# Performance work log

Measured on AMD Instinct MI355X. Metric: run time of the kernel, lower is better.

Reference implementation:

```python
import jax, jax.numpy as jnp
import numpy as np

N, E, D, H, C = 50000, 1600000, 128, 2, 32

def setup_inputs() -> dict:
    key = jax.random.key(0)
    ks = jax.random.split(key, 8)
    x = jax.random.normal(ks[0], (N, D), jnp.float32)
    edge_index = jax.random.randint(ks[1], (2, E), 0, N)
    intra_enrichment_weights = jax.random.uniform(ks[2], (E,), jnp.float32)
    W = jax.random.normal(ks[3], (D, H * C), jnp.float32) * (1.0 / np.sqrt(D))
    att_src = jax.random.normal(ks[4], (H, C), jnp.float32) * 0.1
    att_dst = jax.random.normal(ks[5], (H, C), jnp.float32) * 0.1
    bias = jnp.zeros((H * C,), jnp.float32)
    enrichment_scale = jnp.asarray(0.01, jnp.float32)
    return dict(x=x, edge_index=edge_index,
                intra_enrichment_weights=intra_enrichment_weights,
                W=W, att_src=att_src, att_dst=att_dst, bias=bias,
                enrichment_scale=enrichment_scale)

def reference(x, edge_index, intra_enrichment_weights, W, att_src, att_dst, bias, enrichment_scale):
    n = x.shape[0]
    xf = jax.nn.elu(x)                       # F.elu on input features
    h = (xf @ W).reshape(n, H, C)            # [N, heads, out]
    # GATConv default add_self_loops=True
    loop = jnp.arange(n, dtype=edge_index.dtype)
    src = jnp.concatenate([edge_index[0], loop])
    dst = jnp.concatenate([edge_index[1], loop])
    a_src = jnp.einsum('nhc,hc->nh', h, att_src)   # [N, H]
    a_dst = jnp.einsum('nhc,hc->nh', h, att_dst)
    alpha = jax.nn.leaky_relu(a_src[src] + a_dst[dst], 0.2)  # [E+N, H]
    # softmax over incoming edges per destination node
    m = jax.ops.segment_max(alpha, dst, num_segments=n)
    e = jnp.exp(alpha - m[dst])
    denom = jax.ops.segment_sum(e, dst, num_segments=n)
    p = e / denom[dst]                       # every node has a self-loop -> denom > 0
    out = jax.ops.segment_sum(h[src] * p[:, :, None], dst, num_segments=n)  # [N, H, C]
    out = out.reshape(n, H * C) + bias
    # enrichment bias (scatter-mean of per-edge weights over source nodes)
    s0 = edge_index[0]
    nw = jax.ops.segment_sum(intra_enrichment_weights, s0, num_segments=n)
    cnt = jax.ops.segment_sum(jnp.ones_like(intra_enrichment_weights), s0, num_segments=n)
    nw = nw / jnp.maximum(cnt, 1.0)
    nw = jnp.clip(nw, 0.2, 5.0)
    scale_factor = 0.1 * jax.nn.sigmoid(enrichment_scale)
    return out + scale_factor * (nw[:, None] - 1.0)
```

## Files before the change

kernel.cpp:

```cpp
#include <hip/hip_runtime.h>


typedef unsigned int u32;
typedef unsigned short u16;

#define SLOTS 4864
#define NB_MAX 400
#define EPB 4096

#define XS 136
#define CS 68

#define SMEM_F 43392

typedef __attribute__((ext_vector_type(8))) short short8;
typedef __attribute__((ext_vector_type(4))) float float4v;

__device__ __forceinline__ u16 f2bf(float f) {
    union { float f; u32 u; } v; v.f = f;
    u32 r = v.u + 0x7fffu + ((v.u >> 16) & 1u);
    return (u16)(r >> 16);
}
__device__ __forceinline__ float bf2f(u16 u) {
    union { u32 i; float f; } v; v.i = ((u32)u) << 16; return v.f;
}
__device__ __forceinline__ float bf_lo(u32 u) {
    union { u32 i; float f; } v; v.i = u << 16; return v.f;
}
__device__ __forceinline__ float bf_hi(u32 u) {
    union { u32 i; float f; } v; v.i = u & 0xFFFF0000u; return v.f;
}
__device__ __forceinline__ void bf_split(float v, short& hi, short& lo) {
    u16 h = f2bf(v);
    float hf = bf2f(h);
    hi = (short)h;
    lo = (short)f2bf(v - hf);
}

__global__ void k_prep(const float* __restrict__ Wm,
                       short* __restrict__ Whf, short* __restrict__ Wlf,
                       int* cursA, int* cursB)
{
    int t = threadIdx.x;
    for (int i = t; i < NB_MAX; i += 256) { cursA[i] = 0; cursB[i] = 0; }
    for (int p = t; p < 1024; p += 256) {
        int frag = p >> 6, l = p & 63;
        int ks = frag >> 2, nt = frag & 3;
        int q = l >> 4, m = l & 15;
        int f = nt * 16 + m;
#pragma unroll
        for (int j = 0; j < 8; ++j) {
            int k = ks * 32 + q * 8 + j;
            float wv = Wm[k * 64 + f];
            short hi, lo; bf_split(wv, hi, lo);
            Whf[p * 8 + j] = hi;
            Wlf[p * 8 + j] = lo;
        }
    }
}

static __device__ __forceinline__ void node_body(
    char* smem, int nb_id,
    const float* __restrict__ x,
    const short* __restrict__ Whf, const short* __restrict__ Wlf,
    const float* __restrict__ att_s, const float* __restrict__ att_d,
    u32* __restrict__ hb32, float* __restrict__ a_src, float* __restrict__ a_dst,
    int nN)
{
    short* Ah = (short*)smem;
    short* Al = (short*)(smem + 17408);
    float* Cl = (float*)Ah;

    int t = threadIdx.x;
    int n0 = nb_id * 64;

    for (int j = 0; j < 8; ++j) {
        int idx = t + 256 * j;
        int r = idx >> 5, c4 = idx & 31;
        int gn = n0 + r;
        float4 xv = make_float4(0.f, 0.f, 0.f, 0.f);
        if (gn < nN) xv = ((const float4*)x)[(size_t)gn * 32 + c4];
        float e[4];
        e[0] = xv.x > 0.f ? xv.x : __expf(xv.x) - 1.f;
        e[1] = xv.y > 0.f ? xv.y : __expf(xv.y) - 1.f;
        e[2] = xv.z > 0.f ? xv.z : __expf(xv.z) - 1.f;
        e[3] = xv.w > 0.f ? xv.w : __expf(xv.w) - 1.f;
        short h4[4], l4[4];
#pragma unroll
        for (int i = 0; i < 4; ++i) bf_split(e[i], h4[i], l4[i]);
        *(short4*)&Ah[r * XS + c4 * 4] = make_short4(h4[0], h4[1], h4[2], h4[3]);
        *(short4*)&Al[r * XS + c4 * 4] = make_short4(l4[0], l4[1], l4[2], l4[3]);
    }
    __syncthreads();

    {
        int w = t >> 6, l = t & 63;
        int q = l >> 4, m = l & 15;
        int arow = w * 16 + m;
        float4v acc[4] = {};
#pragma unroll
        for (int ks = 0; ks < 4; ++ks) {
            int k0 = ks * 32 + q * 8;
            short8 ah = *(const short8*)&Ah[arow * XS + k0];
            short8 al = *(const short8*)&Al[arow * XS + k0];
#pragma unroll
            for (int nt = 0; nt < 4; ++nt) {
                short8 bh = *(const short8*)&Whf[((ks * 4 + nt) * 64 + l) * 8];
                short8 bl = *(const short8*)&Wlf[((ks * 4 + nt) * 64 + l) * 8];
                acc[nt] = __builtin_amdgcn_mfma_f32_16x16x32_bf16(ah, bh, acc[nt], 0, 0, 0);
                acc[nt] = __builtin_amdgcn_mfma_f32_16x16x32_bf16(ah, bl, acc[nt], 0, 0, 0);
                acc[nt] = __builtin_amdgcn_mfma_f32_16x16x32_bf16(al, bh, acc[nt], 0, 0, 0);
            }
        }
        __syncthreads();
#pragma unroll
        for (int nt = 0; nt < 4; ++nt)
#pragma unroll
            for (int r = 0; r < 4; ++r)
                Cl[(w * 16 + q * 4 + r) * CS + nt * 16 + m] = acc[nt][r];
    }
    __syncthreads();

    {
        int nl = t >> 2, fq = t & 3;
        int gn = n0 + nl;
        float ps = 0.f, pd = 0.f;
        if (gn < nN) {
            float hv[16];
#pragma unroll
            for (int i = 0; i < 16; ++i) {
                int f = fq * 16 + i;
                hv[i] = Cl[nl * CS + f];
                ps = fmaf(hv[i], att_s[f], ps);
                pd = fmaf(hv[i], att_d[f], pd);
            }
#pragma unroll
            for (int i = 0; i < 8; ++i) {
                u32 pk = ((u32)f2bf(hv[2 * i + 1]) << 16) | (u32)f2bf(hv[2 * i]);
                hb32[(size_t)gn * 32 + fq * 8 + i] = pk;
            }
        }
        float ps2 = ps + __shfl_xor(ps, 1, 64);
        float pd2 = pd + __shfl_xor(pd, 1, 64);
        if (gn < nN && (fq & 1) == 0) {
            a_src[2 * gn + (fq >> 1)] = ps2;
            a_dst[2 * gn + (fq >> 1)] = pd2;
        }
    }
}

static __device__ __forceinline__ void partA_body(
    char* smem, int pa_id,
    const int* __restrict__ ei, const float* __restrict__ wgt,
    int* cursA, int* cursB, u32* bufA, u32* bufB, int E, int nb)
{
    u32* arrA  = (u32*)smem;
    u32* arrB  = (u32*)(smem + 16384);
    int* cntA  = (int*)(smem + 32768);
    int* cntB  = (int*)(smem + 34368);
    int* lofsA = (int*)(smem + 35968);
    int* lofsB = (int*)(smem + 37568);
    int* basA  = (int*)(smem + 39168);
    int* basB  = (int*)(smem + 40768);
    int* part  = (int*)(smem + 42368);

    int t = threadIdx.x;
    for (int b = t; b < nb; b += 256) { cntA[b] = 0; cntB[b] = 0; }
    __syncthreads();

    int base = pa_id * EPB;
    int nv = min(EPB, E - base);
    int sv[16], dv[16]; float wv[16];
#pragma unroll
    for (int k = 0; k < 16; ++k) {
        int e = base + k * 256 + t;
        if (e < E) { sv[k] = ei[e]; dv[k] = ei[E + e]; wv[k] = wgt[e]; }
        else       { sv[k] = -1;    dv[k] = -1;        wv[k] = 0.f; }
    }
#pragma unroll
    for (int k = 0; k < 16; ++k) {
        if (dv[k] >= 0) {
            atomicAdd(&cntA[dv[k] >> 7], 1);
            atomicAdd(&cntB[sv[k] >> 7], 1);
        }
    }
    __syncthreads();
    for (int b = t; b < nb; b += 256) {
        int ca = cntA[b], cb = cntB[b];
        if (ca > 0) basA[b] = atomicAdd(&cursA[b], ca);
        if (cb > 0) basB[b] = atomicAdd(&cursB[b], cb);
    }
    __syncthreads();
    {
        int b0 = 2 * t, b1 = 2 * t + 1;
        int c0 = (b0 < nb) ? cntA[b0] : 0;
        int c1 = (b1 < nb) ? cntA[b1] : 0;
        part[t] = c0 + c1;
        __syncthreads();
        for (int off = 1; off < 256; off <<= 1) {
            int v = (t >= off) ? part[t - off] : 0;
            __syncthreads();
            part[t] += v;
            __syncthreads();
        }
        int excl = part[t] - (c0 + c1);
        if (b0 < nb) lofsA[b0] = excl;
        if (b1 < nb) lofsA[b1] = excl + c0;
        __syncthreads();
        c0 = (b0 < nb) ? cntB[b0] : 0;
        c1 = (b1 < nb) ? cntB[b1] : 0;
        part[t] = c0 + c1;
        __syncthreads();
        for (int off = 1; off < 256; off <<= 1) {
            int v = (t >= off) ? part[t - off] : 0;
            __syncthreads();
            part[t] += v;
            __syncthreads();
        }
        excl = part[t] - (c0 + c1);
        if (b0 < nb) lofsB[b0] = excl;
        if (b1 < nb) lofsB[b1] = excl + c0;
    }
    __syncthreads();
    for (int b = t; b < nb; b += 256) { cntA[b] = 0; cntB[b] = 0; }
    __syncthreads();
#pragma unroll
    for (int k = 0; k < 16; ++k) {
        if (dv[k] >= 0) {
            int bA = dv[k] >> 7;
            int r = lofsA[bA] + atomicAdd(&cntA[bA], 1);
            arrA[r] = ((u32)bA << 23) | ((u32)(dv[k] & 127) << 16) | (u32)sv[k];
            int bB = sv[k] >> 7;
            u32 wf = (u32)(wv[k] * 65536.f);
            if (wf > 0xFFFFu) wf = 0xFFFFu;
            int r2 = lofsB[bB] + atomicAdd(&cntB[bB], 1);
            arrB[r2] = ((u32)bB << 23) | ((u32)(sv[k] & 127) << 16) | wf;
        }
    }
    __syncthreads();
    for (int i = t; i < nv; i += 256) {
        u32 va = arrA[i];
        int bA = va >> 23;
        int g = basA[bA] + (i - lofsA[bA]);
        if (g < SLOTS) bufA[bA * SLOTS + g] = va & 0x7FFFFFu;
        u32 vb = arrB[i];
        int bB = vb >> 23;
        int g2 = basB[bB] + (i - lofsB[bB]);
        if (g2 < SLOTS) bufB[bB * SLOTS + g2] = vb & 0x7FFFFFu;
    }
}

__global__ __launch_bounds__(256) void k_fused(
    const float* __restrict__ x,
    const short* __restrict__ Whf, const short* __restrict__ Wlf,
    const float* __restrict__ att_s, const float* __restrict__ att_d,
    u32* __restrict__ hb32, float* __restrict__ a_src, float* __restrict__ a_dst,
    const int* __restrict__ ei, const float* __restrict__ wgt,
    int* cursA, int* cursB, u32* bufA, u32* bufB,
    int E, int nb, int nblkA, int nN)
{
    __shared__ __align__(16) char smem[SMEM_F];
    int bid = blockIdx.x;
    int q3 = bid / 3;
    if ((bid % 3) == 0 && q3 < nblkA) {
        partA_body(smem, q3, ei, wgt, cursA, cursB, bufA, bufB, E, nb);
    } else {
        int npa_before = min(q3 + ((bid % 3) ? 1 : 0), nblkA);
        node_body(smem, bid - npa_before, x, Whf, Wlf, att_s, att_d,
                  hb32, a_src, a_dst, nN);
    }
}

__global__ __launch_bounds__(1024) void k_final(
    const u32* __restrict__ hb32,
    const float* __restrict__ a_src, const float* __restrict__ a_dst,
    const u32* __restrict__ bufA, const int* __restrict__ cursA,
    const u32* __restrict__ bufB, const int* __restrict__ cursB,
    const float* __restrict__ bias, const float* __restrict__ esc,
    float* __restrict__ out, int nN)
{
    __shared__ u32 st[SLOTS];
    __shared__ u16 st2[SLOTS];
    __shared__ int ldeg[128], lscan[128], lcur[128];
    __shared__ u32 usum[128];
    __shared__ int ucnt[128];

    int b = blockIdx.x, t = threadIdx.x;
    int n0 = b << 7;
    int nA = cursA[b]; if (nA > SLOTS) nA = SLOTS;
    int nB = cursB[b]; if (nB > SLOTS) nB = SLOTS;

    if (t < 128) { ldeg[t] = 0; lcur[t] = 0; usum[t] = 0; ucnt[t] = 0; }
    __syncthreads();
    for (int i = t; i < nA; i += 1024) {
        u32 v = bufA[(size_t)b * SLOTS + i];
        st[i] = v;
        atomicAdd(&ldeg[v >> 16], 1);
    }
    for (int i = t; i < nB; i += 1024) {
        u32 v = bufB[(size_t)b * SLOTS + i];
        atomicAdd(&usum[v >> 16], v & 0xFFFFu);
        atomicAdd(&ucnt[v >> 16], 1);
    }
    __syncthreads();
    if (t < 128) lscan[t] = ldeg[t];
    __syncthreads();
    for (int off = 1; off < 128; off <<= 1) {
        int v = 0;
        if (t < 128 && t >= off) v = lscan[t - off];
        __syncthreads();
        if (t < 128) lscan[t] += v;
        __syncthreads();
    }
    if (t < 128) lscan[t] -= ldeg[t];
    __syncthreads();
    for (int i = t; i < nA; i += 1024) {
        u32 v = st[i];
        int dl = v >> 16;
        int pos = lscan[dl] + atomicAdd(&lcur[dl], 1);
        st2[pos] = (u16)(v & 0xFFFFu);
    }
    __syncthreads();

    int ws = t >> 6, lane = t & 63;
    int q = lane >> 4, fl = lane & 15, head = fl >> 3;
    const uint2* hb2 = (const uint2*)hb32;
    float escv = esc[0];
    float sf = 0.1f / (1.f + __expf(-escv));
    float4 bb = ((const float4*)bias)[fl];

    for (int dl = ws; dl < 128; dl += 16) {
        int gn = n0 + dl;
        if (gn >= nN) break;
        int beg = lscan[dl], cnt = ldeg[dl];
        float2 adv = ((const float2*)a_dst)[gn];
        float2 asv = ((const float2*)a_src)[gn];
        float t0 = asv.x + adv.x; t0 = t0 > 0.f ? t0 : 0.2f * t0;
        float t1 = asv.y + adv.y; t1 = t1 > 0.f ? t1 : 0.2f * t1;
        float es0 = __expf(t0), es1 = __expf(t1);

        float acc0 = 0.f, acc1 = 0.f, acc2 = 0.f, acc3 = 0.f;
        if (q == 0) {
            float eself = head ? es1 : es0;
            uint2 hs = hb2[(size_t)gn * 16 + fl];
            acc0 = eself * bf_lo(hs.x);
            acc1 = eself * bf_hi(hs.x);
            acc2 = eself * bf_lo(hs.y);
            acc3 = eself * bf_hi(hs.y);
        }
        float dsum0 = 0.f, dsum1 = 0.f;

        for (int b0 = 0; b0 < cnt; b0 += 64) {
            int wn = cnt - b0; if (wn > 64) wn = 64;
            u32 si = (u32)gn; float e0 = 0.f, e1 = 0.f;
            if (lane < wn) {
                si = (u32)st2[beg + b0 + lane];
                float2 ap = ((const float2*)a_src)[si];
                float v0 = ap.x + adv.x; v0 = v0 > 0.f ? v0 : 0.2f * v0;
                float v1 = ap.y + adv.y; v1 = v1 > 0.f ? v1 : 0.2f * v1;
                e0 = __expf(v0); e1 = __expf(v1);
            }
            dsum0 += e0; dsum1 += e1;

            int iters = (wn + 3) >> 2;
#pragma unroll 8
            for (int k = 0; k < iters; ++k) {
                int e = 4 * k + q;
                u32 rsi = __shfl(si, e, 64);
                uint2 hv = hb2[(size_t)rsi * 16 + fl];
                float w0 = __shfl(e0, e, 64);
                float w1 = __shfl(e1, e, 64);
                float w = head ? w1 : w0;
                acc0 = fmaf(w, bf_lo(hv.x), acc0);
                acc1 = fmaf(w, bf_hi(hv.x), acc1);
                acc2 = fmaf(w, bf_lo(hv.y), acc2);
                acc3 = fmaf(w, bf_hi(hv.y), acc3);
            }
        }
#pragma unroll
        for (int off = 1; off < 64; off <<= 1) {
            dsum0 += __shfl_xor(dsum0, off, 64);
            dsum1 += __shfl_xor(dsum1, off, 64);
        }
        acc0 += __shfl_xor(acc0, 16, 64); acc0 += __shfl_xor(acc0, 32, 64);
        acc1 += __shfl_xor(acc1, 16, 64); acc1 += __shfl_xor(acc1, 32, 64);
        acc2 += __shfl_xor(acc2, 16, 64); acc2 += __shfl_xor(acc2, 32, 64);
        acc3 += __shfl_xor(acc3, 16, 64); acc3 += __shfl_xor(acc3, 32, 64);

        if (q == 0) {
            float den = (head ? es1 : es0) + (head ? dsum1 : dsum0);
            float inv = 1.f / den;
            float cntf = (float)ucnt[dl];
            float nw = ((float)usum[dl] * (1.f / 65536.f)) / fmaxf(cntf, 1.f);
            nw = fminf(fmaxf(nw, 0.2f), 5.f);
            float en = sf * (nw - 1.f);
            float4 o;
            o.x = acc0 * inv + bb.x + en;
            o.y = acc1 * inv + bb.y + en;
            o.z = acc2 * inv + bb.z + en;
            o.w = acc3 * inv + bb.w + en;
            ((float4*)out)[(size_t)gn * 16 + fl] = o;
        }
    }
}

extern "C" void kernel_launch(void* const* d_in, const int* in_sizes, int n_in,
                              void* d_out, int out_size, void* d_ws, size_t ws_size,
                              hipStream_t stream)
{
    const float* x     = (const float*)d_in[0];
    const int*   ei    = (const int*)d_in[1];
    const float* wgt   = (const float*)d_in[2];
    const float* Wm    = (const float*)d_in[3];
    const float* att_s = (const float*)d_in[4];
    const float* att_d = (const float*)d_in[5];
    const float* bias  = (const float*)d_in[6];
    const float* esc   = (const float*)d_in[7];
    float* out = (float*)d_out;

    int nN = in_sizes[0] / 128;
    int E  = in_sizes[2];
    int NB = (nN + 127) / 128;

    char* p = (char*)d_ws;
    auto alloc = [&](size_t bytes) -> char* {
        char* r = p; p += (bytes + 255) & ~(size_t)255; return r;
    };
    u32*   hb32  = (u32*)  alloc((size_t)nN * 32 * 4);
    float* a_src = (float*)alloc((size_t)nN * 2 * 4);
    float* a_dst = (float*)alloc((size_t)nN * 2 * 4);
    short* Whf   = (short*)alloc(16 * 64 * 8 * 2);
    short* Wlf   = (short*)alloc(16 * 64 * 8 * 2);
    int*   cursA = (int*)  alloc(NB_MAX * 4);
    int*   cursB = (int*)  alloc(NB_MAX * 4);
    u32*   bufA  = (u32*)  alloc((size_t)NB * SLOTS * 4);
    u32*   bufB  = (u32*)  alloc((size_t)NB * SLOTS * 4);

    int nblkA = (E + EPB - 1) / EPB;
    int nblkN = (nN + 63) / 64;
    int nblkF = nblkA + nblkN;

    k_prep<<<dim3(1), dim3(256), 0, stream>>>(Wm, Whf, Wlf, cursA, cursB);
    k_fused<<<dim3(nblkF), dim3(256), 0, stream>>>(x, Whf, Wlf, att_s, att_d,
                                                   hb32, a_src, a_dst,
                                                   ei, wgt, cursA, cursB, bufA, bufB,
                                                   E, NB, nblkA, nN);
    k_final<<<dim3(NB), dim3(1024), 0, stream>>>(hb32, a_src, a_dst, bufA, cursA,
                                                 bufB, cursB, bias, esc, out, nN);
}
```

Before: 178.5 us.

## Replace source-side bucketing with packed global atomics and halve destination bucket size

The per-source enrichment sums are no longer bucketed and scattered through a second buffer. Each edge now does a global atomicAdd into a packed per-node word that holds an 8-bit count and a 24-bit quantized weight sum. Destination buckets shrink from 128 to 64 nodes, so k_final launches twice as many 512-thread blocks with smaller shared memory. Cursors and the packed array are zeroed with a memset. This removes a second scan, scatter and buffer pass, at the cost of 1.6M contended global atomics, and the 8-bit count or 24-bit sum can overflow for nodes with high out-degree.

```diff
diff --git a/kernel.cpp b/kernel.cpp
--- a/kernel.cpp
+++ b/kernel.cpp
@@ -4,14 +4,14 @@
 typedef unsigned int u32;
 typedef unsigned short u16;
 
-#define SLOTS 4864
-#define NB_MAX 400
+#define SLOTS2 2624
+#define NB2_MAX 800
 #define EPB 4096
 
 #define XS 136
 #define CS 68
 
-#define SMEM_F 43392
+#define SMEM_F 34816
 
 typedef __attribute__((ext_vector_type(8))) short short8;
 typedef __attribute__((ext_vector_type(4))) float float4v;
@@ -38,11 +38,9 @@
 }
 
 __global__ void k_prep(const float* __restrict__ Wm,
-                       short* __restrict__ Whf, short* __restrict__ Wlf,
-                       int* cursA, int* cursB)
+                       short* __restrict__ Whf, short* __restrict__ Wlf)
 {
     int t = threadIdx.x;
-    for (int i = t; i < NB_MAX; i += 256) { cursA[i] = 0; cursB[i] = 0; }
     for (int p = t; p < 1024; p += 256) {
         int frag = p >> 6, l = p & 63;
         int ks = frag >> 2, nt = frag & 3;
@@ -152,24 +150,19 @@
 static __device__ __forceinline__ void partA_body(
     char* smem, int pa_id,
     const int* __restrict__ ei, const float* __restrict__ wgt,
-    int* cursA, int* cursB, u32* bufA, u32* bufB, int E, int nb)
+    int* cursA, u32* bufA, u32* nwpack, int E, int nb2)
 {
     u32* arrA  = (u32*)smem;
-    u32* arrB  = (u32*)(smem + 16384);
-    int* cntA  = (int*)(smem + 32768);
-    int* cntB  = (int*)(smem + 34368);
-    int* lofsA = (int*)(smem + 35968);
-    int* lofsB = (int*)(smem + 37568);
-    int* basA  = (int*)(smem + 39168);
-    int* basB  = (int*)(smem + 40768);
-    int* part  = (int*)(smem + 42368);
+    int* cntA  = (int*)(smem + 16384);
+    int* lofsA = (int*)(smem + 19584);
+    int* basA  = (int*)(smem + 22784);
+    int* part  = (int*)(smem + 25984);
 
     int t = threadIdx.x;
-    for (int b = t; b < nb; b += 256) { cntA[b] = 0; cntB[b] = 0; }
+    for (int b = t; b < nb2; b += 256) cntA[b] = 0;
     __syncthreads();
 
     int base = pa_id * EPB;
-    int nv = min(EPB, E - base);
     int sv[16], dv[16]; float wv[16];
 #pragma unroll
     for (int k = 0; k < 16; ++k) {
@@ -180,22 +173,27 @@
 #pragma unroll
     for (int k = 0; k < 16; ++k) {
         if (dv[k] >= 0) {
-            atomicAdd(&cntA[dv[k] >> 7], 1);
-            atomicAdd(&cntB[sv[k] >> 7], 1);
-        }
-    }
-    __syncthreads();
-    for (int b = t; b < nb; b += 256) {
-        int ca = cntA[b], cb = cntB[b];
+            atomicAdd(&cntA[dv[k] >> 6], 1);
+            u32 wq = (u32)(wv[k] * 65536.f);
+            if (wq > 0xFFFFu) wq = 0xFFFFu;
+            atomicAdd(&nwpack[sv[k]], (1u << 24) | wq);
+        }
+    }
+    __syncthreads();
+    for (int b = t; b < nb2; b += 256) {
+        int ca = cntA[b];
         if (ca > 0) basA[b] = atomicAdd(&cursA[b], ca);
-        if (cb > 0) basB[b] = atomicAdd(&cursB[b], cb);
     }
     __syncthreads();
     {
-        int b0 = 2 * t, b1 = 2 * t + 1;
-        int c0 = (b0 < nb) ? cntA[b0] : 0;
-        int c1 = (b1 < nb) ? cntA[b1] : 0;
-        part[t] = c0 + c1;
+        int c[4]; int s = 0;
+#pragma unroll
+        for (int i = 0; i < 4; ++i) {
+            int bb = 4 * t + i;
+            c[i] = (bb < nb2) ? cntA[bb] : 0;
+            s += c[i];
+        }
+        part[t] = s;
         __syncthreads();
         for (int off = 1; off < 256; off <<= 1) {
             int v = (t >= off) ? part[t - off] : 0;
@@ -203,50 +201,32 @@
             part[t] += v;
             __syncthreads();
         }
-        int excl = part[t] - (c0 + c1);
-        if (b0 < nb) lofsA[b0] = excl;
-        if (b1 < nb) lofsA[b1] = excl + c0;
-        __syncthreads();
-        c0 = (b0 < nb) ? cntB[b0] : 0;
-        c1 = (b1 < nb) ? cntB[b1] : 0;
-        part[t] = c0 + c1;
-        __syncthreads();
-        for (int off = 1; off < 256; off <<= 1) {
-            int v = (t >= off) ? part[t - off] : 0;
-            __syncthreads();
-            part[t] += v;
-            __syncthreads();
-        }
-        excl = part[t] - (c0 + c1);
-        if (b0 < nb) lofsB[b0] = excl;
-        if (b1 < nb) lofsB[b1] = excl + c0;
-    }
-    __syncthreads();
-    for (int b = t; b < nb; b += 256) { cntA[b] = 0; cntB[b] = 0; }
+        int excl = part[t] - s;
+#pragma unroll
+        for (int i = 0; i < 4; ++i) {
+            int bb = 4 * t + i;
+            if (bb < nb2) lofsA[bb] = excl;
+            excl += c[i];
+        }
+    }
+    __syncthreads();
+    for (int b = t; b < nb2; b += 256) cntA[b] = 0;
     __syncthreads();
 #pragma unroll
     for (int k = 0; k < 16; ++k) {
         if (dv[k] >= 0) {
-            int bA = dv[k] >> 7;
+            int bA = dv[k] >> 6;
             int r = lofsA[bA] + atomicAdd(&cntA[bA], 1);
-            arrA[r] = ((u32)bA << 23) | ((u32)(dv[k] & 127) << 16) | (u32)sv[k];
-            int bB = sv[k] >> 7;
-            u32 wf = (u32)(wv[k] * 65536.f);
-            if (wf > 0xFFFFu) wf = 0xFFFFu;
-            int r2 = lofsB[bB] + atomicAdd(&cntB[bB], 1);
-            arrB[r2] = ((u32)bB << 23) | ((u32)(sv[k] & 127) << 16) | wf;
-        }
-    }
-    __syncthreads();
+            arrA[r] = ((u32)bA << 22) | ((u32)(dv[k] & 63) << 16) | (u32)sv[k];
+        }
+    }
+    __syncthreads();
+    int nv = min(EPB, E - base);
     for (int i = t; i < nv; i += 256) {
         u32 va = arrA[i];
-        int bA = va >> 23;
+        int bA = va >> 22;
         int g = basA[bA] + (i - lofsA[bA]);
-        if (g < SLOTS) bufA[bA * SLOTS + g] = va & 0x7FFFFFu;
-        u32 vb = arrB[i];
-        int bB = vb >> 23;
-        int g2 = basB[bB] + (i - lofsB[bB]);
-        if (g2 < SLOTS) bufB[bB * SLOTS + g2] = vb & 0x7FFFFFu;
+        if (g < SLOTS2) bufA[bA * SLOTS2 + g] = va & 0x3FFFFFu;
     }
 }
 
@@ -256,14 +236,14 @@
     const float* __restrict__ att_s, const float* __restrict__ att_d,
     u32* __restrict__ hb32, float* __restrict__ a_src, float* __restrict__ a_dst,
     const int* __restrict__ ei, const float* __restrict__ wgt,
-    int* cursA, int* cursB, u32* bufA, u32* bufB,
-    int E, int nb, int nblkA, int nN)
+    int* cursA, u32* bufA, u32* nwpack,
+    int E, int nb2, int nblkA, int nN)
 {
     __shared__ __align__(16) char smem[SMEM_F];
     int bid = blockIdx.x;
     int q3 = bid / 3;
     if ((bid % 3) == 0 && q3 < nblkA) {
-        partA_body(smem, q3, ei, wgt, cursA, cursB, bufA, bufB, E, nb);
+        partA_body(smem, q3, ei, wgt, cursA, bufA, nwpack, E, nb2);
     } else {
         int npa_before = min(q3 + ((bid % 3) ? 1 : 0), nblkA);
         node_body(smem, bid - npa_before, x, Whf, Wlf, att_s, att_d,
@@ -271,50 +251,42 @@
     }
 }
 
-__global__ __launch_bounds__(1024) void k_final(
+__global__ __launch_bounds__(512) void k_final(
     const u32* __restrict__ hb32,
     const float* __restrict__ a_src, const float* __restrict__ a_dst,
     const u32* __restrict__ bufA, const int* __restrict__ cursA,
-    const u32* __restrict__ bufB, const int* __restrict__ cursB,
+    const u32* __restrict__ nwpack,
     const float* __restrict__ bias, const float* __restrict__ esc,
     float* __restrict__ out, int nN)
 {
-    __shared__ u32 st[SLOTS];
-    __shared__ u16 st2[SLOTS];
-    __shared__ int ldeg[128], lscan[128], lcur[128];
-    __shared__ u32 usum[128];
-    __shared__ int ucnt[128];
+    __shared__ u32 st[SLOTS2];
+    __shared__ u16 st2[SLOTS2];
+    __shared__ int ldeg[64], lscan[64], lcur[64];
 
     int b = blockIdx.x, t = threadIdx.x;
-    int n0 = b << 7;
-    int nA = cursA[b]; if (nA > SLOTS) nA = SLOTS;
-    int nB = cursB[b]; if (nB > SLOTS) nB = SLOTS;
-
-    if (t < 128) { ldeg[t] = 0; lcur[t] = 0; usum[t] = 0; ucnt[t] = 0; }
-    __syncthreads();
-    for (int i = t; i < nA; i += 1024) {
-        u32 v = bufA[(size_t)b * SLOTS + i];
+    int n0 = b << 6;
+    int nA = cursA[b]; if (nA > SLOTS2) nA = SLOTS2;
+
+    if (t < 64) { ldeg[t] = 0; lcur[t] = 0; }
+    __syncthreads();
+    for (int i = t; i < nA; i += 512) {
+        u32 v = bufA[(size_t)b * SLOTS2 + i];
         st[i] = v;
         atomicAdd(&ldeg[v >> 16], 1);
     }
-    for (int i = t; i < nB; i += 1024) {
-        u32 v = bufB[(size_t)b * SLOTS + i];
-        atomicAdd(&usum[v >> 16], v & 0xFFFFu);
-        atomicAdd(&ucnt[v >> 16], 1);
-    }
-    __syncthreads();
-    if (t < 128) lscan[t] = ldeg[t];
-    __syncthreads();
-    for (int off = 1; off < 128; off <<= 1) {
+    __syncthreads();
+    if (t < 64) lscan[t] = ldeg[t];
+    __syncthreads();
+    for (int off = 1; off < 64; off <<= 1) {
         int v = 0;
-        if (t < 128 && t >= off) v = lscan[t - off];
+        if (t < 64 && t >= off) v = lscan[t - off];
         __syncthreads();
-        if (t < 128) lscan[t] += v;
+        if (t < 64) lscan[t] += v;
         __syncthreads();
     }
-    if (t < 128) lscan[t] -= ldeg[t];
-    __syncthreads();
-    for (int i = t; i < nA; i += 1024) {
+    if (t < 64) lscan[t] -= ldeg[t];
+    __syncthreads();
+    for (int i = t; i < nA; i += 512) {
         u32 v = st[i];
         int dl = v >> 16;
         int pos = lscan[dl] + atomicAdd(&lcur[dl], 1);
@@ -329,7 +301,7 @@
     float sf = 0.1f / (1.f + __expf(-escv));
     float4 bb = ((const float4*)bias)[fl];
 
-    for (int dl = ws; dl < 128; dl += 16) {
+    for (int dl = ws; dl < 64; dl += 8) {
         int gn = n0 + dl;
         if (gn >= nN) break;
         int beg = lscan[dl], cnt = ldeg[dl];
@@ -390,8 +362,9 @@
         if (q == 0) {
             float den = (head ? es1 : es0) + (head ? dsum1 : dsum0);
             float inv = 1.f / den;
-            float cntf = (float)ucnt[dl];
-            float nw = ((float)usum[dl] * (1.f / 65536.f)) / fmaxf(cntf, 1.f);
+            u32 np = nwpack[gn];
+            float cntf = (float)(np >> 24);
+            float nw = ((float)(np & 0xFFFFFFu) * (1.f / 65536.f)) / fmaxf(cntf, 1.f);
             nw = fminf(fmaxf(nw, 0.2f), 5.f);
             float en = sf * (nw - 1.f);
             float4 o;
@@ -420,7 +393,7 @@
 
     int nN = in_sizes[0] / 128;
     int E  = in_sizes[2];
-    int NB = (nN + 127) / 128;
+    int NB2 = (nN + 63) / 64;
 
     char* p = (char*)d_ws;
     auto alloc = [&](size_t bytes) -> char* {
@@ -431,20 +404,20 @@
     float* a_dst = (float*)alloc((size_t)nN * 2 * 4);
     short* Whf   = (short*)alloc(16 * 64 * 8 * 2);
     short* Wlf   = (short*)alloc(16 * 64 * 8 * 2);
-    int*   cursA = (int*)  alloc(NB_MAX * 4);
-    int*   cursB = (int*)  alloc(NB_MAX * 4);
-    u32*   bufA  = (u32*)  alloc((size_t)NB * SLOTS * 4);
-    u32*   bufB  = (u32*)  alloc((size_t)NB * SLOTS * 4);
+    int*   cursA = (int*)  alloc(NB2_MAX * 4);
+    u32*   nwpack= (u32*)  alloc((size_t)nN * 4);
+    u32*   bufA  = (u32*)  alloc((size_t)NB2 * SLOTS2 * 4);
 
     int nblkA = (E + EPB - 1) / EPB;
     int nblkN = (nN + 63) / 64;
     int nblkF = nblkA + nblkN;
 
-    k_prep<<<dim3(1), dim3(256), 0, stream>>>(Wm, Whf, Wlf, cursA, cursB);
+    hipMemsetAsync(cursA, 0, (size_t)((char*)bufA - (char*)cursA), stream);
+    k_prep<<<dim3(1), dim3(256), 0, stream>>>(Wm, Whf, Wlf);
     k_fused<<<dim3(nblkF), dim3(256), 0, stream>>>(x, Whf, Wlf, att_s, att_d,
                                                    hb32, a_src, a_dst,
-                                                   ei, wgt, cursA, cursB, bufA, bufB,
-                                                   E, NB, nblkA, nN);
-    k_final<<<dim3(NB), dim3(1024), 0, stream>>>(hb32, a_src, a_dst, bufA, cursA,
-                                                 bufB, cursB, bias, esc, out, nN);
-}
+                                                   ei, wgt, cursA, bufA, nwpack,
+                                                   E, NB2, nblkA, nN);
+    k_final<<<dim3(NB2), dim3(512), 0, stream>>>(hb32, a_src, a_dst, bufA, cursA,
+                                                 nwpack, bias, esc, out, nN);
+}
```

Measured after the change: 228.2 us. 1.28x slower.
